# Performance work log

Measured on AMD Instinct MI355X. Metric: run time of the kernel, lower is better.

## Reference

```python
import jax, jax.numpy as jnp
import numpy as np

DIM = 384
NUM_HEADS = 12
HEAD_DIM = DIM // NUM_HEADS  # 32
N = 361  # 19x19 Go board
EPS = 1e-6


def setup_inputs() -> dict:
    key = jax.random.key(0)
    ks = jax.random.split(key, 8)
    B = 128
    x = jax.random.normal(ks[0], (B, DIM, 19, 19), dtype=jnp.float32)
    s = 1.0 / np.sqrt(DIM)
    q_w = jax.random.normal(ks[1], (DIM, DIM), dtype=jnp.float32) * s
    k_w = jax.random.normal(ks[2], (DIM, DIM), dtype=jnp.float32) * s
    v_w = jax.random.normal(ks[3], (DIM, DIM), dtype=jnp.float32) * s
    out_w = jax.random.normal(ks[4], (DIM, DIM), dtype=jnp.float32) * s
    norm_w = jnp.ones((DIM,), dtype=jnp.float32)
    theta = jax.random.uniform(ks[5], (N, HEAD_DIM), dtype=jnp.float32) * (2.0 * np.pi)
    cos_t = jnp.cos(theta)
    sin_t = jnp.sin(theta)
    return {"x": x, "q_w": q_w, "k_w": k_w, "v_w": v_w, "out_w": out_w,
            "norm_w": norm_w, "cos_t": cos_t, "sin_t": sin_t}


def _rmsnorm(x, w):
    rms = jnp.sqrt(jnp.mean(x * x, axis=-1, keepdims=True) + EPS)
    return w * (x / rms)


def _rope(x, cos_t, sin_t):
    # x: [B, N, H, D]; interleaved pairing (0,1),(2,3),...
    B, Np, H, D = x.shape
    xp = x.reshape(B, Np, H, D // 2, 2)
    rot = jnp.stack([-xp[..., 1], xp[..., 0]], axis=-1).reshape(B, Np, H, D)
    cos = cos_t[None, :, None, :]
    sin = sin_t[None, :, None, :]
    return x * cos + rot * sin


def reference(x, q_w, k_w, v_w, out_w, norm_w, cos_t, sin_t):
    B, C, Hh, Ww = x.shape
    Np = Hh * Ww  # 361
    x_flat = x.reshape(B, C, Np).transpose(0, 2, 1)  # [B, N, C]
    residual = x_flat.astype(jnp.float32)
    xn = _rmsnorm(residual, norm_w)
    # torch stores weight = W.T and applies x @ weight.T == x @ W
    q = (xn @ q_w).reshape(B, Np, NUM_HEADS, HEAD_DIM)
    k = (xn @ k_w).reshape(B, Np, NUM_HEADS, HEAD_DIM)
    v = (xn @ v_w).reshape(B, Np, NUM_HEADS, HEAD_DIM)
    q = _rope(q, cos_t, sin_t)
    k = _rope(k, cos_t, sin_t)
    scale = 1.0 / np.sqrt(HEAD_DIM)
    attn = jnp.einsum('bnhd,bmhd->bhnm', q, k) * scale  # [B, H, N, N]
    attn = jax.nn.softmax(attn, axis=-1)
    out = jnp.einsum('bhnm,bmhd->bnhd', attn, v).reshape(B, Np, DIM)
    out = out @ out_w
    return (residual + out).astype(x.dtype)  # [B, N, C]
```

## Files before the change

### kernel.cpp

```cpp
#include <hip/hip_runtime.h>
#include <hip/hip_bf16.h>

typedef float f32x4 __attribute__((ext_vector_type(4)));
typedef __bf16 bf16x8 __attribute__((ext_vector_type(8)));

#define NPOS 361
#define NBATCH 128
#define M_TOT (NBATCH * NPOS)

__global__ __launch_bounds__(256) void prep_w_kernel(
    const float* __restrict__ qw, const float* __restrict__ kw,
    const float* __restrict__ vw, const float* __restrict__ ow,
    __hip_bfloat16* __restrict__ wqkvt, __hip_bfloat16* __restrict__ owt) {
  int idx = blockIdx.x * 256 + threadIdx.x;
  const int TOT1 = 1152 * 384;
  if (idx < TOT1) {
    int n = idx / 384, kk = idx % 384;
    const float* src = (n < 384) ? qw : (n < 768 ? kw : vw);
    int nn = n % 384;
    wqkvt[idx] = __float2bfloat16(src[kk * 384 + nn]);
  } else if (idx < TOT1 + 384 * 384) {
    int j = idx - TOT1;
    int n = j / 384, kk = j % 384;
    owt[j] = __float2bfloat16(ow[kk * 384 + n]);
  }
}

__global__ __launch_bounds__(256) void rms_t_kernel(
    const float* __restrict__ x, const float* __restrict__ nw,
    __hip_bfloat16* __restrict__ xn) {
  int b = blockIdx.x / 12, nt = blockIdx.x % 12;
  int n0 = nt * 32;
  __shared__ float xt[384][33];
  int tid = threadIdx.x;
  const float* xb = x + (size_t)b * (384 * 361);
  for (int idx = tid; idx < 384 * 32; idx += 256) {
    int c = idx >> 5, j = idx & 31;
    float v = 0.f;
    int n = n0 + j;
    if (n < 361) v = xb[c * 361 + n];
    xt[c][j] = v;
  }
  __syncthreads();
  int lane = tid & 63, wid = tid >> 6;
  for (int j = wid; j < 32; j += 4) {
    int n = n0 + j;
    if (n >= 361) break;
    float vals[6];
    float ss = 0.f;
#pragma unroll
    for (int i = 0; i < 6; ++i) { vals[i] = xt[lane + i * 64][j]; ss += vals[i] * vals[i]; }
#pragma unroll
    for (int off = 1; off < 64; off <<= 1) ss += __shfl_xor(ss, off);
    float inv = rsqrtf(ss * (1.f / 384.f) + 1e-6f);
    size_t row = (size_t)b * 361 + n;
#pragma unroll
    for (int i = 0; i < 6; ++i) {
      int c = lane + i * 64;
      xn[row * 384 + c] = __float2bfloat16(vals[i] * inv * nw[c]);
    }
  }
}

__global__ __launch_bounds__(256) void qkv_gemm_kernel(
    const __hip_bfloat16* __restrict__ A, const __hip_bfloat16* __restrict__ BT,
    __hip_bfloat16* __restrict__ qkv) {
  const int m0 = blockIdx.x * 128;
  const int n0 = blockIdx.y * 128;
  __shared__ __hip_bfloat16 As[128][40];
  __shared__ __hip_bfloat16 Bs[128][40];
  const int tid = threadIdx.x;
  const int lane = tid & 63, wid = tid >> 6;
  const int wr = wid >> 1, wc = wid & 1;
  const int cB = lane & 15, koff = (lane >> 4) * 8;
  f32x4 acc[4][4] = {};
  for (int k0 = 0; k0 < 384; k0 += 32) {
    __syncthreads();
    {
      int row = tid >> 2, c8 = (tid & 3) * 8;
      *reinterpret_cast<bf16x8*>(&As[row][c8]) =
          *reinterpret_cast<const bf16x8*>(&A[(size_t)(m0 + row) * 384 + k0 + c8]);
      *reinterpret_cast<bf16x8*>(&Bs[row][c8]) =
          *reinterpret_cast<const bf16x8*>(&BT[(size_t)(n0 + row) * 384 + k0 + c8]);
      row += 64;
      *reinterpret_cast<bf16x8*>(&As[row][c8]) =
          *reinterpret_cast<const bf16x8*>(&A[(size_t)(m0 + row) * 384 + k0 + c8]);
      *reinterpret_cast<bf16x8*>(&Bs[row][c8]) =
          *reinterpret_cast<const bf16x8*>(&BT[(size_t)(n0 + row) * 384 + k0 + c8]);
    }
    __syncthreads();
    bf16x8 af[4], bfr[4];
#pragma unroll
    for (int i = 0; i < 4; ++i)
      af[i] = *reinterpret_cast<const bf16x8*>(&As[wr * 64 + i * 16 + cB][koff]);
#pragma unroll
    for (int j = 0; j < 4; ++j)
      bfr[j] = *reinterpret_cast<const bf16x8*>(&Bs[wc * 64 + j * 16 + cB][koff]);
#pragma unroll
    for (int i = 0; i < 4; ++i)
#pragma unroll
      for (int j = 0; j < 4; ++j)
        acc[i][j] = __builtin_amdgcn_mfma_f32_16x16x32_bf16(af[i], bfr[j], acc[i][j], 0, 0, 0);
  }
  const int rg = lane >> 4;
  const int sel = n0 / 384;
  __hip_bfloat16* dst = qkv + (size_t)sel * M_TOT * 384;
#pragma unroll
  for (int i = 0; i < 4; ++i)
#pragma unroll
    for (int j = 0; j < 4; ++j) {
      int cc = n0 - sel * 384 + wc * 64 + j * 16 + cB;
#pragma unroll
      for (int r = 0; r < 4; ++r) {
        int row = m0 + wr * 64 + i * 16 + rg * 4 + r;
        dst[(size_t)row * 384 + cc] = __float2bfloat16(acc[i][j][r]);
      }
    }
}

__global__ __launch_bounds__(256) void rope_kernel(
    __hip_bfloat16* __restrict__ qk, const float* __restrict__ cost,
    const float* __restrict__ sint) {
  size_t idx = (size_t)blockIdx.x * 256 + threadIdx.x;
  const size_t TOT = (size_t)2 * M_TOT * 192;
  if (idx >= TOT) return;
  int p = (int)(idx % 192);
  size_t row = idx / 192;
  int n = (int)(row % 361);
  int dp = p & 15, h = p >> 4;
  __hip_bfloat16* ptr = qk + row * 384 + h * 32 + dp * 2;
  float x0 = __bfloat162float(ptr[0]);
  float x1 = __bfloat162float(ptr[1]);
  int ci = n * 32 + dp * 2;
  float c0 = cost[ci], s0 = sint[ci];
  float c1 = cost[ci + 1], s1 = sint[ci + 1];
  ptr[0] = __float2bfloat16(x0 * c0 - x1 * s0);
  ptr[1] = __float2bfloat16(x1 * c1 + x0 * s1);
}

__global__ __launch_bounds__(512) void attn_kernel(
    const __hip_bfloat16* __restrict__ q, const __hip_bfloat16* __restrict__ k,
    const __hip_bfloat16* __restrict__ v, __hip_bfloat16* __restrict__ o) {
  const int b = blockIdx.x / 12, h = blockIdx.x % 12;
  __shared__ __hip_bfloat16 Ks[368][40];
  __shared__ __hip_bfloat16 VT[32][392];
  __shared__ __hip_bfloat16 Pb[8][16][40];
  const int tid = threadIdx.x, lane = tid & 63, wid = tid >> 6;
  const size_t base = ((size_t)b * 361) * 384 + (size_t)h * 32;
  const __hip_bfloat16* qb = q + base;
  const __hip_bfloat16* kb = k + base;
  const __hip_bfloat16* vb = v + base;
  for (int idx = tid; idx < 368 * 4; idx += 512) {
    int m = idx >> 2, c8 = (idx & 3) * 8;
    int mc = m < 361 ? m : 360;
    *reinterpret_cast<bf16x8*>(&Ks[m][c8]) =
        *reinterpret_cast<const bf16x8*>(&kb[(size_t)mc * 384 + c8]);
  }
  for (int idx = tid; idx < 384 * 32; idx += 512) {
    int m = idx >> 5, d = idx & 31;
    float val = (m < 361) ? __bfloat162float(vb[(size_t)m * 384 + d]) : 0.f;
    VT[d][m] = __float2bfloat16(val);
  }
  __syncthreads();
  const int cB = lane & 15, rg = lane >> 4, koff = rg * 8;
  const float scale = 0.17677669529663688f;
  for (int rt = wid; rt < 23; rt += 8) {
    int qrow = rt * 16 + cB;
    if (qrow > 360) qrow = 360;
    bf16x8 af = *reinterpret_cast<const bf16x8*>(&qb[(size_t)qrow * 384 + koff]);
    f32x4 S[23];
#pragma unroll
    for (int mt = 0; mt < 23; ++mt) {
      bf16x8 bfr = *reinterpret_cast<const bf16x8*>(&Ks[mt * 16 + cB][koff]);
      f32x4 z = {};
      S[mt] = __builtin_amdgcn_mfma_f32_16x16x32_bf16(af, bfr, z, 0, 0, 0);
    }
    float mx[4] = {-1e30f, -1e30f, -1e30f, -1e30f};
#pragma unroll
    for (int mt = 0; mt < 23; ++mt)
#pragma unroll
      for (int r = 0; r < 4; ++r) {
        float s = S[mt][r] * scale;
        if (mt == 22 && cB >= 9) s = -1e30f;
        S[mt][r] = s;
        mx[r] = fmaxf(mx[r], s);
      }
#pragma unroll
    for (int off = 1; off < 16; off <<= 1)
#pragma unroll
      for (int r = 0; r < 4; ++r) mx[r] = fmaxf(mx[r], __shfl_xor(mx[r], off));
    float sum[4] = {0.f, 0.f, 0.f, 0.f};
#pragma unroll
    for (int mt = 0; mt < 23; ++mt)
#pragma unroll
      for (int r = 0; r < 4; ++r) {
        float pv = __expf(S[mt][r] - mx[r]);
        S[mt][r] = pv;
        sum[r] += pv;
      }
#pragma unroll
    for (int off = 1; off < 16; off <<= 1)
#pragma unroll
      for (int r = 0; r < 4; ++r) sum[r] += __shfl_xor(sum[r], off);
    f32x4 O0 = {}, O1 = {};
#pragma unroll
    for (int km = 0; km < 12; ++km) {
#pragma unroll
      for (int t2 = 0; t2 < 2; ++t2) {
        int mt = km * 2 + t2;
#pragma unroll
        for (int r = 0; r < 4; ++r) {
          float pv = (mt < 23) ? S[mt][r] : 0.f;
          Pb[wid][rg * 4 + r][t2 * 16 + cB] = __float2bfloat16(pv);
        }
      }
      bf16x8 pa = *reinterpret_cast<const bf16x8*>(&Pb[wid][cB][koff]);
      bf16x8 bv0 = *reinterpret_cast<const bf16x8*>(&VT[cB][km * 32 + koff]);
      bf16x8 bv1 = *reinterpret_cast<const bf16x8*>(&VT[16 + cB][km * 32 + koff]);
      O0 = __builtin_amdgcn_mfma_f32_16x16x32_bf16(pa, bv0, O0, 0, 0, 0);
      O1 = __builtin_amdgcn_mfma_f32_16x16x32_bf16(pa, bv1, O1, 0, 0, 0);
    }
#pragma unroll
    for (int r = 0; r < 4; ++r) {
      int n = rt * 16 + rg * 4 + r;
      if (n < 361) {
        float is = 1.f / sum[r];
        o[base + (size_t)n * 384 + cB] = __float2bfloat16(O0[r] * is);
        o[base + (size_t)n * 384 + 16 + cB] = __float2bfloat16(O1[r] * is);
      }
    }
  }
}

__global__ __launch_bounds__(256) void out_gemm_kernel(
    const __hip_bfloat16* __restrict__ A, const __hip_bfloat16* __restrict__ BT,
    const float* __restrict__ x, float* __restrict__ out) {
  const int m0 = blockIdx.x * 128;
  const int n0 = blockIdx.y * 128;
  __shared__ __hip_bfloat16 As[128][40];
  __shared__ __hip_bfloat16 Bs[128][40];
  const int tid = threadIdx.x;
  const int lane = tid & 63, wid = tid >> 6;
  const int wr = wid >> 1, wc = wid & 1;
  const int cB = lane & 15, koff = (lane >> 4) * 8;
  f32x4 acc[4][4] = {};
  for (int k0 = 0; k0 < 384; k0 += 32) {
    __syncthreads();
    {
      int row = tid >> 2, c8 = (tid & 3) * 8;
      *reinterpret_cast<bf16x8*>(&As[row][c8]) =
          *reinterpret_cast<const bf16x8*>(&A[(size_t)(m0 + row) * 384 + k0 + c8]);
      *reinterpret_cast<bf16x8*>(&Bs[row][c8]) =
          *reinterpret_cast<const bf16x8*>(&BT[(size_t)(n0 + row) * 384 + k0 + c8]);
      row += 64;
      *reinterpret_cast<bf16x8*>(&As[row][c8]) =
          *reinterpret_cast<const bf16x8*>(&A[(size_t)(m0 + row) * 384 + k0 + c8]);
      *reinterpret_cast<bf16x8*>(&Bs[row][c8]) =
          *reinterpret_cast<const bf16x8*>(&BT[(size_t)(n0 + row) * 384 + k0 + c8]);
    }
    __syncthreads();
    bf16x8 af[4], bfr[4];
#pragma unroll
    for (int i = 0; i < 4; ++i)
      af[i] = *reinterpret_cast<const bf16x8*>(&As[wr * 64 + i * 16 + cB][koff]);
#pragma unroll
    for (int j = 0; j < 4; ++j)
      bfr[j] = *reinterpret_cast<const bf16x8*>(&Bs[wc * 64 + j * 16 + cB][koff]);
#pragma unroll
    for (int i = 0; i < 4; ++i)
#pragma unroll
      for (int j = 0; j < 4; ++j)
        acc[i][j] = __builtin_amdgcn_mfma_f32_16x16x32_bf16(af[i], bfr[j], acc[i][j], 0, 0, 0);
  }
  const int rg = lane >> 4;
#pragma unroll
  for (int i = 0; i < 4; ++i)
#pragma unroll
    for (int j = 0; j < 4; ++j) {
      int col = n0 + wc * 64 + j * 16 + cB;
#pragma unroll
      for (int r = 0; r < 4; ++r) {
        int row = m0 + wr * 64 + i * 16 + rg * 4 + r;
        int bb = row / 361;
        int n = row - bb * 361;
        float res = x[((size_t)bb * 384 + col) * 361 + n];
        out[(size_t)row * 384 + col] = acc[i][j][r] + res;
      }
    }
}

extern "C" void kernel_launch(void* const* d_in, const int* in_sizes, int n_in,
                              void* d_out, int out_size, void* d_ws, size_t ws_size,
                              hipStream_t stream) {
  const float* x    = (const float*)d_in[0];
  const float* qw   = (const float*)d_in[1];
  const float* kw   = (const float*)d_in[2];
  const float* vw   = (const float*)d_in[3];
  const float* ow   = (const float*)d_in[4];
  const float* nw   = (const float*)d_in[5];
  const float* cost = (const float*)d_in[6];
  const float* sint = (const float*)d_in[7];
  float* out = (float*)d_out;
  char* ws = (char*)d_ws;

  const size_t SZ_XN = (size_t)M_TOT * 384 * 2;
  __hip_bfloat16* xn    = (__hip_bfloat16*)(ws);
  __hip_bfloat16* qkv   = (__hip_bfloat16*)(ws + SZ_XN);
  __hip_bfloat16* wqkvt = (__hip_bfloat16*)(ws + SZ_XN * 4);
  __hip_bfloat16* owt   = (__hip_bfloat16*)(ws + SZ_XN * 4 + 1152 * 384 * 2);
  __hip_bfloat16* ao    = xn;

  prep_w_kernel<<<2304, 256, 0, stream>>>(qw, kw, vw, ow, wqkvt, owt);
  rms_t_kernel<<<128 * 12, 256, 0, stream>>>(x, nw, xn);
  qkv_gemm_kernel<<<dim3(361, 9), 256, 0, stream>>>(xn, wqkvt, qkv);
  {
    size_t tot = (size_t)2 * M_TOT * 192;
    int blocks = (int)((tot + 255) / 256);
    rope_kernel<<<blocks, 256, 0, stream>>>(qkv, cost, sint);
  }
  attn_kernel<<<128 * 12, 512, 0, stream>>>(qkv, qkv + (size_t)M_TOT * 384,
                                            qkv + (size_t)2 * M_TOT * 384, ao);
  out_gemm_kernel<<<dim3(361, 3), 256, 0, stream>>>(ao, owt, x, out);
}
```

Measured before the change: 510.1 us.

## Use direct global-to-LDS loads in GEMMs, XCD-aware tile mapping, vectorize prep kernels

GEMM tile staging now uses global_load_lds 16-byte direct loads into unpadded LDS tiles, so the data no longer passes through registers. Workgroup ids are remapped so consecutive tiles land on the same XCD, which should improve L2 reuse. The weight transpose uses a shared-memory tile for coalesced access, and rmsnorm stores are vectorized from a row-major LDS buffer. Dropping the LDS padding risks bank conflicts on the fragment reads.

```diff
diff --git a/kernel.cpp b/kernel.cpp
--- a/kernel.cpp
+++ b/kernel.cpp
@@ -7,22 +7,34 @@
 #define NPOS 361
 #define NBATCH 128
 #define M_TOT (NBATCH * NPOS)
+
+__device__ inline void gload16(const void* g, void* l) {
+  __builtin_amdgcn_global_load_lds(
+      (const __attribute__((address_space(1))) void*)g,
+      (__attribute__((address_space(3))) void*)l, 16, 0, 0);
+}
 
 __global__ __launch_bounds__(256) void prep_w_kernel(
     const float* __restrict__ qw, const float* __restrict__ kw,
     const float* __restrict__ vw, const float* __restrict__ ow,
     __hip_bfloat16* __restrict__ wqkvt, __hip_bfloat16* __restrict__ owt) {
-  int idx = blockIdx.x * 256 + threadIdx.x;
-  const int TOT1 = 1152 * 384;
-  if (idx < TOT1) {
-    int n = idx / 384, kk = idx % 384;
-    const float* src = (n < 384) ? qw : (n < 768 ? kw : vw);
-    int nn = n % 384;
-    wqkvt[idx] = __float2bfloat16(src[kk * 384 + nn]);
-  } else if (idx < TOT1 + 384 * 384) {
-    int j = idx - TOT1;
-    int n = j / 384, kk = j % 384;
-    owt[j] = __float2bfloat16(ow[kk * 384 + n]);
+  int bid = blockIdx.x;
+  int si = bid / 144, t = bid % 144;
+  int tr = (t / 12) * 32, tc = (t % 12) * 32;
+  const float* src = si == 0 ? qw : si == 1 ? kw : si == 2 ? vw : ow;
+  __hip_bfloat16* dst = si < 3 ? wqkvt + si * 147456 : owt;
+  __shared__ float tile[32][33];
+  int c = threadIdx.x & 31, r0 = threadIdx.x >> 5;
+#pragma unroll
+  for (int i = 0; i < 4; ++i) {
+    int r = r0 + i * 8;
+    tile[r][c] = src[(size_t)(tr + r) * 384 + tc + c];
+  }
+  __syncthreads();
+#pragma unroll
+  for (int i = 0; i < 4; ++i) {
+    int r = r0 + i * 8;
+    dst[(size_t)(tc + r) * 384 + tr + c] = __float2bfloat16(tile[c][r]);
   }
 }
 
@@ -31,71 +43,72 @@
     __hip_bfloat16* __restrict__ xn) {
   int b = blockIdx.x / 12, nt = blockIdx.x % 12;
   int n0 = nt * 32;
-  __shared__ float xt[384][33];
+  __shared__ float xt[32 * 388];
   int tid = threadIdx.x;
   const float* xb = x + (size_t)b * (384 * 361);
   for (int idx = tid; idx < 384 * 32; idx += 256) {
-    int c = idx >> 5, j = idx & 31;
-    float v = 0.f;
+    int j = idx & 31, c = idx >> 5;
     int n = n0 + j;
-    if (n < 361) v = xb[c * 361 + n];
-    xt[c][j] = v;
+    xt[j * 388 + c] = (n < 361) ? xb[c * 361 + n] : 0.f;
   }
   __syncthreads();
   int lane = tid & 63, wid = tid >> 6;
   for (int j = wid; j < 32; j += 4) {
     int n = n0 + j;
     if (n >= 361) break;
-    float vals[6];
-    float ss = 0.f;
-#pragma unroll
-    for (int i = 0; i < 6; ++i) { vals[i] = xt[lane + i * 64][j]; ss += vals[i] * vals[i]; }
+    const float* row = &xt[j * 388];
+    f32x4 v4 = *(const f32x4*)&row[lane * 4];
+    float va = row[256 + 2 * lane], vb2 = row[256 + 2 * lane + 1];
+    float ss = v4[0] * v4[0] + v4[1] * v4[1] + v4[2] * v4[2] + v4[3] * v4[3] +
+               va * va + vb2 * vb2;
 #pragma unroll
     for (int off = 1; off < 64; off <<= 1) ss += __shfl_xor(ss, off);
     float inv = rsqrtf(ss * (1.f / 384.f) + 1e-6f);
-    size_t row = (size_t)b * 361 + n;
-#pragma unroll
-    for (int i = 0; i < 6; ++i) {
-      int c = lane + i * 64;
-      xn[row * 384 + c] = __float2bfloat16(vals[i] * inv * nw[c]);
-    }
+    f32x4 w4 = *(const f32x4*)&nw[lane * 4];
+    float wa = nw[256 + 2 * lane], wb = nw[256 + 2 * lane + 1];
+    size_t rowo = ((size_t)b * 361 + n) * 384;
+    __hip_bfloat162 p0 = __float22bfloat162_rn({v4[0] * inv * w4[0], v4[1] * inv * w4[1]});
+    __hip_bfloat162 p1 = __float22bfloat162_rn({v4[2] * inv * w4[2], v4[3] * inv * w4[3]});
+    __hip_bfloat162 p2 = __float22bfloat162_rn({va * inv * wa, vb2 * inv * wb});
+    *(__hip_bfloat162*)&xn[rowo + lane * 4] = p0;
+    *(__hip_bfloat162*)&xn[rowo + lane * 4 + 2] = p1;
+    *(__hip_bfloat162*)&xn[rowo + 256 + 2 * lane] = p2;
   }
 }
 
 __global__ __launch_bounds__(256) void qkv_gemm_kernel(
     const __hip_bfloat16* __restrict__ A, const __hip_bfloat16* __restrict__ BT,
     __hip_bfloat16* __restrict__ qkv) {
-  const int m0 = blockIdx.x * 128;
-  const int n0 = blockIdx.y * 128;
-  __shared__ __hip_bfloat16 As[128][40];
-  __shared__ __hip_bfloat16 Bs[128][40];
-  const int tid = threadIdx.x;
-  const int lane = tid & 63, wid = tid >> 6;
+  const int nwg = 361 * 9;
+  int orig = blockIdx.x;
+  int xcd = orig & 7, loc = orig >> 3;
+  const int q8 = nwg >> 3, r8 = nwg & 7;
+  int wgid = (xcd < r8 ? xcd * (q8 + 1) : r8 * (q8 + 1) + (xcd - r8) * q8) + loc;
+  const int mt = wgid / 9, nt = wgid % 9;
+  const int m0 = mt * 128, n0 = nt * 128;
+  __shared__ __hip_bfloat16 As[128 * 32];
+  __shared__ __hip_bfloat16 Bs[128 * 32];
+  const int tid = threadIdx.x, lane = tid & 63, wid = tid >> 6;
   const int wr = wid >> 1, wc = wid & 1;
   const int cB = lane & 15, koff = (lane >> 4) * 8;
+  const int rS0 = wid * 32 + (lane >> 2);
+  const int rS1 = rS0 + 16;
+  const int cby = (lane & 3) * 16;
   f32x4 acc[4][4] = {};
   for (int k0 = 0; k0 < 384; k0 += 32) {
     __syncthreads();
-    {
-      int row = tid >> 2, c8 = (tid & 3) * 8;
-      *reinterpret_cast<bf16x8*>(&As[row][c8]) =
-          *reinterpret_cast<const bf16x8*>(&A[(size_t)(m0 + row) * 384 + k0 + c8]);
-      *reinterpret_cast<bf16x8*>(&Bs[row][c8]) =
-          *reinterpret_cast<const bf16x8*>(&BT[(size_t)(n0 + row) * 384 + k0 + c8]);
-      row += 64;
-      *reinterpret_cast<bf16x8*>(&As[row][c8]) =
-          *reinterpret_cast<const bf16x8*>(&A[(size_t)(m0 + row) * 384 + k0 + c8]);
-      *reinterpret_cast<bf16x8*>(&Bs[row][c8]) =
-          *reinterpret_cast<const bf16x8*>(&BT[(size_t)(n0 + row) * 384 + k0 + c8]);
-    }
+    gload16((const char*)(A + (size_t)(m0 + rS0) * 384 + k0) + cby, As + wid * 1024);
+    gload16((const char*)(A + (size_t)(m0 + rS1) * 384 + k0) + cby, As + wid * 1024 + 512);
+    gload16((const char*)(BT + (size_t)(n0 + rS0) * 384 + k0) + cby, Bs + wid * 1024);
+    gload16((const char*)(BT + (size_t)(n0 + rS1) * 384 + k0) + cby, Bs + wid * 1024 + 512);
     __syncthreads();
     bf16x8 af[4], bfr[4];
 #pragma unroll
     for (int i = 0; i < 4; ++i)
-      af[i] = *reinterpret_cast<const bf16x8*>(&As[wr * 64 + i * 16 + cB][koff]);
+      af[i] = *reinterpret_cast<const bf16x8*>(&As[(wr * 64 + i * 16 + cB) * 32 + koff]);
 #pragma unroll
     for (int j = 0; j < 4; ++j)
-      bfr[j] = *reinterpret_cast<const bf16x8*>(&Bs[wc * 64 + j * 16 + cB][koff]);
+      bfr[j] = *reinterpret_cast<const bf16x8*>(&Bs[(wc * 64 + j * 16 + cB) * 32 + koff]);
 #pragma unroll
     for (int i = 0; i < 4; ++i)
 #pragma unroll
@@ -235,37 +248,36 @@
 __global__ __launch_bounds__(256) void out_gemm_kernel(
     const __hip_bfloat16* __restrict__ A, const __hip_bfloat16* __restrict__ BT,
     const float* __restrict__ x, float* __restrict__ out) {
-  const int m0 = blockIdx.x * 128;
-  const int n0 = blockIdx.y * 128;
-  __shared__ __hip_bfloat16 As[128][40];
-  __shared__ __hip_bfloat16 Bs[128][40];
-  const int tid = threadIdx.x;
-  const int lane = tid & 63, wid = tid >> 6;
+  const int nwg = 361 * 3;
+  int orig = blockIdx.x;
+  int xcd = orig & 7, loc = orig >> 3;
+  const int q8 = nwg >> 3, r8 = nwg & 7;
+  int wgid = (xcd < r8 ? xcd * (q8 + 1) : r8 * (q8 + 1) + (xcd - r8) * q8) + loc;
+  const int mt = wgid / 3, nt = wgid % 3;
+  const int m0 = mt * 128, n0 = nt * 128;
+  __shared__ __hip_bfloat16 As[128 * 32];
+  __shared__ __hip_bfloat16 Bs[128 * 32];
+  const int tid = threadIdx.x, lane = tid & 63, wid = tid >> 6;
   const int wr = wid >> 1, wc = wid & 1;
   const int cB = lane & 15, koff = (lane >> 4) * 8;
+  const int rS0 = wid * 32 + (lane >> 2);
+  const int rS1 = rS0 + 16;
+  const int cby = (lane & 3) * 16;
   f32x4 acc[4][4] = {};
   for (int k0 = 0; k0 < 384; k0 += 32) {
     __syncthreads();
-    {
-      int row = tid >> 2, c8 = (tid & 3) * 8;
-      *reinterpret_cast<bf16x8*>(&As[row][c8]) =
-          *reinterpret_cast<const bf16x8*>(&A[(size_t)(m0 + row) * 384 + k0 + c8]);
-      *reinterpret_cast<bf16x8*>(&Bs[row][c8]) =
-          *reinterpret_cast<const bf16x8*>(&BT[(size_t)(n0 + row) * 384 + k0 + c8]);
-      row += 64;
-      *reinterpret_cast<bf16x8*>(&As[row][c8]) =
-          *reinterpret_cast<const bf16x8*>(&A[(size_t)(m0 + row) * 384 + k0 + c8]);
-      *reinterpret_cast<bf16x8*>(&Bs[row][c8]) =
-          *reinterpret_cast<const bf16x8*>(&BT[(size_t)(n0 + row) * 384 + k0 + c8]);
-    }
+    gload16((const char*)(A + (size_t)(m0 + rS0) * 384 + k0) + cby, As + wid * 1024);
+    gload16((const char*)(A + (size_t)(m0 + rS1) * 384 + k0) + cby, As + wid * 1024 + 512);
+    gload16((const char*)(BT + (size_t)(n0 + rS0) * 384 + k0) + cby, Bs + wid * 1024);
+    gload16((const char*)(BT + (size_t)(n0 + rS1) * 384 + k0) + cby, Bs + wid * 1024 + 512);
     __syncthreads();
     bf16x8 af[4], bfr[4];
 #pragma unroll
     for (int i = 0; i < 4; ++i)
-      af[i] = *reinterpret_cast<const bf16x8*>(&As[wr * 64 + i * 16 + cB][koff]);
+      af[i] = *reinterpret_cast<const bf16x8*>(&As[(wr * 64 + i * 16 + cB) * 32 + koff]);
 #pragma unroll
     for (int j = 0; j < 4; ++j)
-      bfr[j] = *reinterpret_cast<const bf16x8*>(&Bs[wc * 64 + j * 16 + cB][koff]);
+      bfr[j] = *reinterpret_cast<const bf16x8*>(&Bs[(wc * 64 + j * 16 + cB) * 32 + koff]);
 #pragma unroll
     for (int i = 0; i < 4; ++i)
 #pragma unroll
@@ -310,9 +322,9 @@
   __hip_bfloat16* owt   = (__hip_bfloat16*)(ws + SZ_XN * 4 + 1152 * 384 * 2);
   __hip_bfloat16* ao    = xn;
 
-  prep_w_kernel<<<2304, 256, 0, stream>>>(qw, kw, vw, ow, wqkvt, owt);
+  prep_w_kernel<<<576, 256, 0, stream>>>(qw, kw, vw, ow, wqkvt, owt);
   rms_t_kernel<<<128 * 12, 256, 0, stream>>>(x, nw, xn);
-  qkv_gemm_kernel<<<dim3(361, 9), 256, 0, stream>>>(xn, wqkvt, qkv);
+  qkv_gemm_kernel<<<361 * 9, 256, 0, stream>>>(xn, wqkvt, qkv);
   {
     size_t tot = (size_t)2 * M_TOT * 192;
     int blocks = (int)((tot + 255) / 256);
@@ -320,5 +332,5 @@
   }
   attn_kernel<<<128 * 12, 512, 0, stream>>>(qkv, qkv + (size_t)M_TOT * 384,
                                             qkv + (size_t)2 * M_TOT * 384, ao);
-  out_gemm_kernel<<<dim3(361, 3), 256, 0, stream>>>(ao, owt, x, out);
-}
+  out_gemm_kernel<<<361 * 3, 256, 0, stream>>>(ao, owt, x, out);
+}
```

Result: faster. 467.5 us (-8.4%).
